# Kernel tuning notes

Measured on AMD Instinct MI355X. Metric: run time of the kernel, lower is better.

The kernel has to match this reference:

```python
import jax, jax.numpy as jnp
import numpy as np

EPS = 1e-6

def rmsnorm(x, w):
    # x: (B, N, D), w: (D,)
    var = jnp.mean(jnp.square(x), axis=-1, keepdims=True)
    return x * jax.lax.rsqrt(var + EPS) * w

def head_mixing(x):
    # Parameter-free cross-head mix: split each head's D dims into N chunks
    # and transpose the (head, chunk) axes. x: (B, N, D), D % N == 0.
    B, N, D = x.shape
    c = D // N
    return x.reshape(B, N, N, c).transpose(0, 2, 1, 3).reshape(B, N, D)

def setup_inputs() -> dict:
    key = jax.random.key(0)
    ks = jax.random.split(key, 4)
    B, N, D, H = 8192, 16, 256, 512
    return {
        "x": jax.random.normal(ks[0], (B, N, D), dtype=jnp.float32),
        "norm1_w": jnp.ones((D,), dtype=jnp.float32),
        "norm2_w": jnp.ones((D,), dtype=jnp.float32),
        "w1": jax.random.normal(ks[1], (N, D, H), dtype=jnp.float32) * (1.0 / np.sqrt(D)),
        "w3": jax.random.normal(ks[2], (N, D, H), dtype=jnp.float32) * (1.0 / np.sqrt(D)),
        "w2": jax.random.normal(ks[3], (N, H, D), dtype=jnp.float32) * (1.0 / np.sqrt(H)),
    }

def reference(x, norm1_w, norm2_w, w1, w3, w2):
    # P = HeadMixing(RMSNorm(X)) + X
    p = head_mixing(rmsnorm(x, norm1_w)) + x
    # Q = PerHeadSwiGLUFFN(RMSNorm(P)) + P  (grouped per-head SwiGLU)
    pn = rmsnorm(p, norm2_w)                       # (B, N, D)
    g = jnp.einsum('bnd,ndh->bnh', pn, w1)         # gate proj
    u = jnp.einsum('bnd,ndh->bnh', pn, w3)         # up proj
    h = jax.nn.silu(g) * u                         # (B, N, H)
    q = jnp.einsum('bnh,nhd->bnd', h, w2) + p
    return q
```

## Files before the change

kernel.cpp:

```cpp
#include <hip/hip_runtime.h>
#include <hip/hip_bf16.h>

#define B_ 8192
#define N_ 16
#define D_ 256
#define H_ 512

using bf16x8 = __attribute__((ext_vector_type(8))) short;
using f32x4  = __attribute__((ext_vector_type(4))) float;

__device__ __forceinline__ void gload_lds16(const void* g, void* l) {
    __builtin_amdgcn_global_load_lds(
        (const __attribute__((address_space(1))) void*)g,
        (__attribute__((address_space(3))) void*)l, 16, 0, 0);
}

__device__ __forceinline__ short f2bf(float f) {
    unsigned int u = __float_as_uint(f);
    u += 0x7fffu + ((u >> 16) & 1u);
    return (short)(u >> 16);
}

__device__ __forceinline__ float bf2f(short s) {
    return __uint_as_float(((unsigned int)(unsigned short)s) << 16);
}

__device__ __forceinline__ unsigned int pack2(float lo, float hi) {
    return (unsigned int)(unsigned short)f2bf(lo)
         | ((unsigned int)(unsigned short)f2bf(hi) << 16);
}

__device__ __forceinline__ f32x4 mfma(bf16x8 a, bf16x8 b, f32x4 c) {
    return __builtin_amdgcn_mfma_f32_16x16x32_bf16(a, b, c, 0, 0, 0);
}

__device__ __forceinline__ bf16x8 rd64(const short* base, int row, int g) {
    int gp = (g ^ row) & 7;
    return *(const bf16x8*)&base[(row << 6) + (gp << 3)];
}

template<int NT>
__device__ __forceinline__ void gemmc(const short* __restrict__ Ag, int sA,
                                      const short* __restrict__ Bg, int sB,
                                      short* As, short* Bs,
                                      f32x4 (&acc)[4][4],
                                      int t, int rowA0, int rowB0) {
    int lane = t & 63;
    int l16 = lane & 15, kq = lane >> 4;

#pragma unroll 1
    for (int kt = 0; kt < NT; ++kt) {
        int k0 = kt * 64;
#pragma unroll
        for (int rnd = 0; rnd < 4; ++rnd) {
            int flat = rnd * 256 + t;
            int row = flat >> 3, g = flat & 7;
            int sg = (g ^ row) & 7;
            gload_lds16(Ag + (size_t)row * sA + k0 + sg * 8, As + flat * 8);
        }
#pragma unroll
        for (int rnd = 0; rnd < 4; ++rnd) {
            int flat = rnd * 256 + t;
            int row = flat >> 3, g = flat & 7;
            int sg = (g ^ row) & 7;
            gload_lds16(Bg + (size_t)row * sB + k0 + sg * 8, Bs + flat * 8);
        }
        __syncthreads();

#pragma unroll
        for (int kh = 0; kh < 2; ++kh) {
            int g = kh * 4 + kq;
            bf16x8 aF[4], bF[4];
#pragma unroll
            for (int j = 0; j < 4; ++j)
                bF[j] = rd64(Bs, rowB0 + j * 16 + l16, g);
#pragma unroll
            for (int i = 0; i < 4; ++i)
                aF[i] = rd64(As, rowA0 + i * 16 + l16, g);
#pragma unroll
            for (int i = 0; i < 4; ++i)
#pragma unroll
                for (int j = 0; j < 4; ++j)
                    acc[i][j] = mfma(aF[i], bF[j], acc[i][j]);
        }
        __syncthreads();
    }
}

__global__ __launch_bounds__(256) void k_prep(const float* __restrict__ w1,
                                              const float* __restrict__ w3,
                                              const float* __restrict__ w2,
                                              short* __restrict__ wgu,
                                              short* __restrict__ w2t) {
    int o = blockIdx.x * 256 + threadIdx.x;
    int n = o >> 17;
    int r = o & 131071;
    int h = r >> 8, d = r & 255;
    size_t base = ((size_t)n * 1024 + (h >> 4) * 32 + (h & 15)) * 256 + d;
    wgu[base]            = f2bf(w1[(size_t)n * 131072 + (size_t)d * 512 + h]);
    wgu[base + 16 * 256] = f2bf(w3[(size_t)n * 131072 + (size_t)d * 512 + h]);
    int d2 = r >> 9, h2 = r & 511;
    w2t[o] = f2bf(w2[(size_t)n * 131072 + (size_t)h2 * 256 + d2]);
}

__global__ __launch_bounds__(256) void k_mix(const float* __restrict__ x,
                                             const float* __restrict__ n1w,
                                             const float* __restrict__ n2w,
                                             unsigned int* __restrict__ pb_u,
                                             unsigned int* __restrict__ pn_u) {
    __shared__ __align__(16) float xs[N_ * D_];
    __shared__ __align__(16) float ps[N_ * D_];
    __shared__ float inv1[N_];
    __shared__ float inv2[N_];
    int b = blockIdx.x;
    int t = threadIdx.x;
    int w = t >> 6, lane = t & 63;

    const float4* xb4 = (const float4*)(x + (size_t)b * (N_ * D_));
    float4* xs4 = (float4*)xs;
    float4* ps4 = (float4*)ps;
#pragma unroll
    for (int i = 0; i < 4; ++i) xs4[t + i * 256] = xb4[t + i * 256];
    __syncthreads();

#pragma unroll
    for (int q = 0; q < 4; ++q) {
        int row = w * 4 + q;
        float4 v = xs4[row * 64 + lane];
        float s = v.x * v.x + v.y * v.y + v.z * v.z + v.w * v.w;
        s += __shfl_xor(s, 1);  s += __shfl_xor(s, 2);
        s += __shfl_xor(s, 4);  s += __shfl_xor(s, 8);
        s += __shfl_xor(s, 16); s += __shfl_xor(s, 32);
        if (lane == 0) inv1[row] = rsqrtf(s * (1.0f / 256.0f) + 1e-6f);
    }
    __syncthreads();

    {
        int n = t >> 4, j = t & 15;
        float i1 = inv1[n];
#pragma unroll 1
        for (int m = 0; m < 16; ++m) {
            float v = xs[n * 256 + m * 16 + j] * i1 * n1w[m * 16 + j]
                    + xs[m * 256 + t];
            ps[m * 256 + t] = v;
        }
    }
    __syncthreads();

#pragma unroll
    for (int q = 0; q < 4; ++q) {
        int row = w * 4 + q;
        float4 v = ps4[row * 64 + lane];
        float s = v.x * v.x + v.y * v.y + v.z * v.z + v.w * v.w;
        s += __shfl_xor(s, 1);  s += __shfl_xor(s, 2);
        s += __shfl_xor(s, 4);  s += __shfl_xor(s, 8);
        s += __shfl_xor(s, 16); s += __shfl_xor(s, 32);
        if (lane == 0) inv2[row] = rsqrtf(s * (1.0f / 256.0f) + 1e-6f);
    }
    __syncthreads();

    int dh = t & 127, mh = t >> 7;
    float wA = n2w[2 * dh], wB = n2w[2 * dh + 1];
#pragma unroll
    for (int i = 0; i < 8; ++i) {
        int m = mh * 8 + i;
        float2 f = *(const float2*)&ps[m * 256 + 2 * dh];
        float iv = inv2[m];
        size_t off = ((size_t)m * B_ + b) * (D_ / 2) + dh;
        pb_u[off] = pack2(f.x, f.y);
        pn_u[off] = pack2(f.x * iv * wA, f.y * iv * wB);
    }
}

__global__ __launch_bounds__(256, 4) void k_gu(const short* __restrict__ pn,
                                               const short* __restrict__ wgu,
                                               short* __restrict__ hact) {
    __shared__ __align__(16) short As[128 * 64];
    __shared__ __align__(16) short Bs[128 * 64];

    int bid = blockIdx.x;
    int bx = (bid & 7) * 1024 + (bid >> 3);
    int head = bx >> 9;
    int mt = (bx >> 3) & 63;
    int nt = bx & 7;

    int t = threadIdx.x;
    int w = t >> 6, lane = t & 63;
    int l16 = lane & 15, kq = lane >> 4;
    int wm = w >> 1, wn = w & 1;

    f32x4 acc[4][4];
#pragma unroll
    for (int i = 0; i < 4; ++i)
#pragma unroll
        for (int j = 0; j < 4; ++j) acc[i][j] = (f32x4){0.f, 0.f, 0.f, 0.f};

    const short* Ag = pn  + ((size_t)head * B_ + (size_t)mt * 128) * D_;
    const short* Bg = wgu + ((size_t)head * 1024 + (size_t)nt * 128) * D_;

    gemmc<4>(Ag, D_, Bg, D_, As, Bs, acc, t, wm * 64, wn * 64);

    size_t hb = (size_t)head * B_ * H_;
#pragma unroll
    for (int mf = 0; mf < 4; ++mf) {
        int m = mt * 128 + wm * 64 + mf * 16 + kq * 4;
#pragma unroll
        for (int p = 0; p < 2; ++p) {
            int h = nt * 64 + (wn * 2 + p) * 16 + l16;
#pragma unroll
            for (int r = 0; r < 4; ++r) {
                float g = acc[mf][2 * p][r];
                float u = acc[mf][2 * p + 1][r];
                float hv = g * (1.0f / (1.0f + __expf(-g))) * u;
                hact[hb + (size_t)(m + r) * H_ + h] = f2bf(hv);
            }
        }
    }
}

__global__ __launch_bounds__(256, 4) void k_dn(const short* __restrict__ hact,
                                               const short* __restrict__ w2t,
                                               const short* __restrict__ pb,
                                               float* __restrict__ out) {
    __shared__ __align__(16) short As[128 * 64];
    __shared__ __align__(16) short Bs[128 * 64];

    int bid = blockIdx.x;
    int bx = (bid & 7) * 256 + (bid >> 3);
    int head = bx >> 7;
    int mt = (bx >> 1) & 63;
    int nt = bx & 1;

    int t = threadIdx.x;
    int w = t >> 6, lane = t & 63;
    int l16 = lane & 15, kq = lane >> 4;
    int wm = w >> 1, wn = w & 1;

    f32x4 acc[4][4];
#pragma unroll
    for (int i = 0; i < 4; ++i)
#pragma unroll
        for (int j = 0; j < 4; ++j) acc[i][j] = (f32x4){0.f, 0.f, 0.f, 0.f};

    const short* Ag = hact + ((size_t)head * B_ + (size_t)mt * 128) * H_;
    const short* Bg = w2t  + ((size_t)head * D_ + (size_t)nt * 128) * H_;

    gemmc<8>(Ag, H_, Bg, H_, As, Bs, acc, t, wm * 64, wn * 64);

#pragma unroll
    for (int mf = 0; mf < 4; ++mf) {
        int m = mt * 128 + wm * 64 + mf * 16 + kq * 4;
#pragma unroll
        for (int nf = 0; nf < 4; ++nf) {
            int d = nt * 128 + wn * 64 + nf * 16 + l16;
#pragma unroll
            for (int r = 0; r < 4; ++r) {
                float v = acc[mf][nf][r]
                        + bf2f(pb[((size_t)head * B_ + m + r) * D_ + d]);
                out[(size_t)(m + r) * (N_ * D_) + head * D_ + d] = v;
            }
        }
    }
}

extern "C" void kernel_launch(void* const* d_in, const int* in_sizes, int n_in,
                              void* d_out, int out_size, void* d_ws, size_t ws_size,
                              hipStream_t stream) {
    const float* x   = (const float*)d_in[0];
    const float* n1w = (const float*)d_in[1];
    const float* n2w = (const float*)d_in[2];
    const float* w1  = (const float*)d_in[3];
    const float* w3  = (const float*)d_in[4];
    const float* w2  = (const float*)d_in[5];
    float* out = (float*)d_out;

    char* ws = (char*)d_ws;
    short* wgu  = (short*)(ws);
    short* w2t  = (short*)(ws + (8ull   << 20));
    short* pn   = (short*)(ws + (12ull  << 20));
    short* pb   = (short*)(ws + (76ull  << 20));
    short* hact = (short*)(ws + (140ull << 20));

    k_prep<<<(N_ * D_ * H_) / 256, 256, 0, stream>>>(w1, w3, w2, wgu, w2t);
    k_mix<<<B_, 256, 0, stream>>>(x, n1w, n2w,
                                  (unsigned int*)pb, (unsigned int*)pn);
    k_gu<<<N_ * (B_ / 128) * (1024 / 128), 256, 0, stream>>>(pn, wgu, hact);
    k_dn<<<N_ * (B_ / 128) * (D_ / 128), 256, 0, stream>>>(hact, w2t, pb, out);
}
```

Before: 286.0 us.

## Keep A tile resident in k_gu, double-buffer k_dn, stagger mix LDS access

k_gu now loads the full 128x256 activation tile into LDS once and loops over all 8 N-tiles of the gate/up weights, so the A operand is not re-fetched per output tile. k_dn gets double-buffered LDS staging so the next K-slice's global loads overlap the current MFMAs. k_mix rotates its chunk index per thread group to reduce LDS bank conflicts. Dynamic LDS grows to 80KB and 64KB, and launch bounds drop to 2 blocks per CU, which lowers occupancy and cuts k_gu's grid to 1024 blocks, each running a serial loop.

```diff
diff --git a/kernel.cpp b/kernel.cpp
--- a/kernel.cpp
+++ b/kernel.cpp
@@ -34,56 +34,21 @@
     return __builtin_amdgcn_mfma_f32_16x16x32_bf16(a, b, c, 0, 0, 0);
 }
 
-__device__ __forceinline__ bf16x8 rd64(const short* base, int row, int g) {
-    int gp = (g ^ row) & 7;
-    return *(const bf16x8*)&base[(row << 6) + (gp << 3)];
-}
-
-template<int NT>
-__device__ __forceinline__ void gemmc(const short* __restrict__ Ag, int sA,
-                                      const short* __restrict__ Bg, int sB,
-                                      short* As, short* Bs,
-                                      f32x4 (&acc)[4][4],
-                                      int t, int rowA0, int rowB0) {
-    int lane = t & 63;
-    int l16 = lane & 15, kq = lane >> 4;
-
-#pragma unroll 1
-    for (int kt = 0; kt < NT; ++kt) {
-        int k0 = kt * 64;
-#pragma unroll
-        for (int rnd = 0; rnd < 4; ++rnd) {
-            int flat = rnd * 256 + t;
-            int row = flat >> 3, g = flat & 7;
-            int sg = (g ^ row) & 7;
-            gload_lds16(Ag + (size_t)row * sA + k0 + sg * 8, As + flat * 8);
-        }
-#pragma unroll
-        for (int rnd = 0; rnd < 4; ++rnd) {
-            int flat = rnd * 256 + t;
-            int row = flat >> 3, g = flat & 7;
-            int sg = (g ^ row) & 7;
-            gload_lds16(Bg + (size_t)row * sB + k0 + sg * 8, Bs + flat * 8);
-        }
-        __syncthreads();
-
-#pragma unroll
-        for (int kh = 0; kh < 2; ++kh) {
-            int g = kh * 4 + kq;
-            bf16x8 aF[4], bF[4];
-#pragma unroll
-            for (int j = 0; j < 4; ++j)
-                bF[j] = rd64(Bs, rowB0 + j * 16 + l16, g);
-#pragma unroll
-            for (int i = 0; i < 4; ++i)
-                aF[i] = rd64(As, rowA0 + i * 16 + l16, g);
-#pragma unroll
-            for (int i = 0; i < 4; ++i)
-#pragma unroll
-                for (int j = 0; j < 4; ++j)
-                    acc[i][j] = mfma(aF[i], bF[j], acc[i][j]);
-        }
-        __syncthreads();
+template<int GR>
+__device__ __forceinline__ bf16x8 rdg(const short* base, int row, int g) {
+    int gp = (g & ~7) | ((g ^ row) & 7);
+    return *(const bf16x8*)&base[row * GR * 8 + gp * 8];
+}
+
+template<int S>
+__device__ __forceinline__ void stage64(const short* __restrict__ gsrc, int k0,
+                                        short* lds, int t) {
+#pragma unroll
+    for (int rnd = 0; rnd < 4; ++rnd) {
+        int flat = rnd * 256 + t;
+        int row = flat >> 3, g = flat & 7;
+        int sg = (g ^ row) & 7;
+        gload_lds16(gsrc + (size_t)row * S + k0 + sg * 8, lds + flat * 8);
     }
 }
 
@@ -140,9 +105,10 @@
         float i1 = inv1[n];
 #pragma unroll 1
         for (int m = 0; m < 16; ++m) {
-            float v = xs[n * 256 + m * 16 + j] * i1 * n1w[m * 16 + j]
-                    + xs[m * 256 + t];
-            ps[m * 256 + t] = v;
+            int mm = (m + n) & 15;
+            float v = xs[n * 256 + mm * 16 + j] * i1 * n1w[mm * 16 + j]
+                    + xs[mm * 256 + t];
+            ps[mm * 256 + t] = v;
         }
     }
     __syncthreads();
@@ -172,58 +138,93 @@
     }
 }
 
-__global__ __launch_bounds__(256, 4) void k_gu(const short* __restrict__ pn,
+__global__ __launch_bounds__(256, 2) void k_gu(const short* __restrict__ pn,
                                                const short* __restrict__ wgu,
                                                short* __restrict__ hact) {
-    __shared__ __align__(16) short As[128 * 64];
-    __shared__ __align__(16) short Bs[128 * 64];
+    extern __shared__ short sm[];
+    short* As = sm;
+    short* Bs = sm + 32768;
 
     int bid = blockIdx.x;
-    int bx = (bid & 7) * 1024 + (bid >> 3);
-    int head = bx >> 9;
-    int mt = (bx >> 3) & 63;
-    int nt = bx & 7;
+    int bx = (bid & 7) * 128 + (bid >> 3);
+    int head = bx >> 6;
+    int mt = bx & 63;
 
     int t = threadIdx.x;
     int w = t >> 6, lane = t & 63;
     int l16 = lane & 15, kq = lane >> 4;
     int wm = w >> 1, wn = w & 1;
-
-    f32x4 acc[4][4];
-#pragma unroll
-    for (int i = 0; i < 4; ++i)
-#pragma unroll
-        for (int j = 0; j < 4; ++j) acc[i][j] = (f32x4){0.f, 0.f, 0.f, 0.f};
-
-    const short* Ag = pn  + ((size_t)head * B_ + (size_t)mt * 128) * D_;
-    const short* Bg = wgu + ((size_t)head * 1024 + (size_t)nt * 128) * D_;
-
-    gemmc<4>(Ag, D_, Bg, D_, As, Bs, acc, t, wm * 64, wn * 64);
+    int rowA0 = wm * 64, rowB0 = wn * 64;
+
+    const short* Ag = pn + ((size_t)head * B_ + (size_t)mt * 128) * D_;
+
+#pragma unroll
+    for (int rnd = 0; rnd < 16; ++rnd) {
+        int flat = rnd * 256 + t;
+        int row = flat >> 5, g = flat & 31;
+        int sg = (g & ~7) | ((g ^ row) & 7);
+        gload_lds16(Ag + (size_t)row * D_ + sg * 8, As + flat * 8);
+    }
 
     size_t hb = (size_t)head * B_ * H_;
-#pragma unroll
-    for (int mf = 0; mf < 4; ++mf) {
-        int m = mt * 128 + wm * 64 + mf * 16 + kq * 4;
-#pragma unroll
-        for (int p = 0; p < 2; ++p) {
-            int h = nt * 64 + (wn * 2 + p) * 16 + l16;
-#pragma unroll
-            for (int r = 0; r < 4; ++r) {
-                float g = acc[mf][2 * p][r];
-                float u = acc[mf][2 * p + 1][r];
-                float hv = g * (1.0f / (1.0f + __expf(-g))) * u;
-                hact[hb + (size_t)(m + r) * H_ + h] = f2bf(hv);
+
+#pragma unroll 1
+    for (int nt = 0; nt < 8; ++nt) {
+        const short* Bg = wgu + ((size_t)head * 1024 + (size_t)nt * 128) * D_;
+
+        f32x4 acc[4][4];
+#pragma unroll
+        for (int i = 0; i < 4; ++i)
+#pragma unroll
+            for (int j = 0; j < 4; ++j) acc[i][j] = (f32x4){0.f, 0.f, 0.f, 0.f};
+
+#pragma unroll
+        for (int kt = 0; kt < 4; ++kt) {
+            stage64<256>(Bg, kt * 64, Bs, t);
+            __syncthreads();
+#pragma unroll
+            for (int kh = 0; kh < 2; ++kh) {
+                int gB = kh * 4 + kq;
+                int gA = kt * 8 + kh * 4 + kq;
+                bf16x8 aF[4], bF[4];
+#pragma unroll
+                for (int j = 0; j < 4; ++j)
+                    bF[j] = rdg<8>(Bs, rowB0 + j * 16 + l16, gB);
+#pragma unroll
+                for (int i = 0; i < 4; ++i)
+                    aF[i] = rdg<32>(As, rowA0 + i * 16 + l16, gA);
+#pragma unroll
+                for (int i = 0; i < 4; ++i)
+#pragma unroll
+                    for (int j = 0; j < 4; ++j)
+                        acc[i][j] = mfma(aF[i], bF[j], acc[i][j]);
             }
-        }
-    }
-}
-
-__global__ __launch_bounds__(256, 4) void k_dn(const short* __restrict__ hact,
+            __syncthreads();
+        }
+
+#pragma unroll
+        for (int mf = 0; mf < 4; ++mf) {
+            int m = mt * 128 + wm * 64 + mf * 16 + kq * 4;
+#pragma unroll
+            for (int p = 0; p < 2; ++p) {
+                int h = nt * 64 + (wn * 2 + p) * 16 + l16;
+#pragma unroll
+                for (int r = 0; r < 4; ++r) {
+                    float g = acc[mf][2 * p][r];
+                    float u = acc[mf][2 * p + 1][r];
+                    float hv = g * (1.0f / (1.0f + __expf(-g))) * u;
+                    hact[hb + (size_t)(m + r) * H_ + h] = f2bf(hv);
+                }
+            }
+        }
+    }
+}
+
+__global__ __launch_bounds__(256, 2) void k_dn(const short* __restrict__ hact,
                                                const short* __restrict__ w2t,
                                                const short* __restrict__ pb,
                                                float* __restrict__ out) {
-    __shared__ __align__(16) short As[128 * 64];
-    __shared__ __align__(16) short Bs[128 * 64];
+    extern __shared__ short sm[];
 
     int bid = blockIdx.x;
     int bx = (bid & 7) * 256 + (bid >> 3);
@@ -235,6 +236,7 @@
     int w = t >> 6, lane = t & 63;
     int l16 = lane & 15, kq = lane >> 4;
     int wm = w >> 1, wn = w & 1;
+    int rowA0 = wm * 64, rowB0 = wn * 64;
 
     f32x4 acc[4][4];
 #pragma unroll
@@ -245,7 +247,36 @@
     const short* Ag = hact + ((size_t)head * B_ + (size_t)mt * 128) * H_;
     const short* Bg = w2t  + ((size_t)head * D_ + (size_t)nt * 128) * H_;
 
-    gemmc<8>(Ag, H_, Bg, H_, As, Bs, acc, t, wm * 64, wn * 64);
+    stage64<512>(Ag, 0, sm, t);
+    stage64<512>(Bg, 0, sm + 16384, t);
+    __syncthreads();
+
+#pragma unroll
+    for (int kt = 0; kt < 8; ++kt) {
+        short* Asl = sm + (kt & 1) * 8192;
+        short* Bsl = sm + 16384 + (kt & 1) * 8192;
+        if (kt < 7) {
+            stage64<512>(Ag, (kt + 1) * 64, sm + ((kt + 1) & 1) * 8192, t);
+            stage64<512>(Bg, (kt + 1) * 64, sm + 16384 + ((kt + 1) & 1) * 8192, t);
+        }
+#pragma unroll
+        for (int kh = 0; kh < 2; ++kh) {
+            int g = kh * 4 + kq;
+            bf16x8 aF[4], bF[4];
+#pragma unroll
+            for (int j = 0; j < 4; ++j)
+                bF[j] = rdg<8>(Bsl, rowB0 + j * 16 + l16, g);
+#pragma unroll
+            for (int i = 0; i < 4; ++i)
+                aF[i] = rdg<8>(Asl, rowA0 + i * 16 + l16, g);
+#pragma unroll
+            for (int i = 0; i < 4; ++i)
+#pragma unroll
+                for (int j = 0; j < 4; ++j)
+                    acc[i][j] = mfma(aF[i], bF[j], acc[i][j]);
+        }
+        __syncthreads();
+    }
 
 #pragma unroll
     for (int mf = 0; mf < 4; ++mf) {
@@ -281,9 +312,14 @@
     short* pb   = (short*)(ws + (76ull  << 20));
     short* hact = (short*)(ws + (140ull << 20));
 
+    (void)hipFuncSetAttribute((const void*)k_gu,
+                              hipFuncAttributeMaxDynamicSharedMemorySize, 81920);
+    (void)hipFuncSetAttribute((const void*)k_dn,
+                              hipFuncAttributeMaxDynamicSharedMemorySize, 65536);
+
     k_prep<<<(N_ * D_ * H_) / 256, 256, 0, stream>>>(w1, w3, w2, wgu, w2t);
     k_mix<<<B_, 256, 0, stream>>>(x, n1w, n2w,
                                   (unsigned int*)pb, (unsigned int*)pn);
-    k_gu<<<N_ * (B_ / 128) * (1024 / 128), 256, 0, stream>>>(pn, wgu, hact);
-    k_dn<<<N_ * (B_ / 128) * (D_ / 128), 256, 0, stream>>>(hact, w2t, pb, out);
-}
+    k_gu<<<N_ * (B_ / 128), 256, 81920, stream>>>(pn, wgu, hact);
+    k_dn<<<N_ * (B_ / 128) * (D_ / 128), 256, 65536, stream>>>(hact, w2t, pb, out);
+}
```

Measured after the change: 318.4 us. 11.3% more time.

## Widen GEMM tiles to 128x256 with 512-thread blocks for gate-up and down projections

Applied to the files above, without the earlier changes.

Both GEMM kernels now use 512-thread blocks (8 waves) computing 128x256 output tiles instead of 256-thread blocks computing 128x128. The A tile is staged once per block and reused across twice as many output columns, halving global reads of activations and the number of blocks. The K loop is also fully unrolled with compile-time strides. LDS use grows to 48KB per block, which may lower occupancy, and the down projection grid shrinks to 1024 blocks.

```diff
diff --git a/kernel.cpp b/kernel.cpp
--- a/kernel.cpp
+++ b/kernel.cpp
@@ -34,37 +34,37 @@
     return __builtin_amdgcn_mfma_f32_16x16x32_bf16(a, b, c, 0, 0, 0);
 }
 
-__device__ __forceinline__ bf16x8 rd64(const short* base, int row, int g) {
+__device__ __forceinline__ bf16x8 rdp(const short* base, int row, int g) {
     int gp = (g ^ row) & 7;
     return *(const bf16x8*)&base[(row << 6) + (gp << 3)];
 }
 
-template<int NT>
-__device__ __forceinline__ void gemmc(const short* __restrict__ Ag, int sA,
-                                      const short* __restrict__ Bg, int sB,
+template<int ROWS, int S>
+__device__ __forceinline__ void stage512(const short* __restrict__ gsrc,
+                                         int k0, short* lds, int t) {
+#pragma unroll
+    for (int rnd = 0; rnd < ROWS / 64; ++rnd) {
+        int flat = rnd * 512 + t;
+        int row = flat >> 3, g = flat & 7;
+        int sg = (g ^ row) & 7;
+        gload_lds16(gsrc + (size_t)row * S + k0 + sg * 8, lds + flat * 8);
+    }
+}
+
+template<int NT, int SA, int SB>
+__device__ __forceinline__ void gemmw(const short* __restrict__ Ag,
+                                      const short* __restrict__ Bg,
                                       short* As, short* Bs,
                                       f32x4 (&acc)[4][4],
                                       int t, int rowA0, int rowB0) {
     int lane = t & 63;
     int l16 = lane & 15, kq = lane >> 4;
 
-#pragma unroll 1
+#pragma unroll
     for (int kt = 0; kt < NT; ++kt) {
-        int k0 = kt * 64;
-#pragma unroll
-        for (int rnd = 0; rnd < 4; ++rnd) {
-            int flat = rnd * 256 + t;
-            int row = flat >> 3, g = flat & 7;
-            int sg = (g ^ row) & 7;
-            gload_lds16(Ag + (size_t)row * sA + k0 + sg * 8, As + flat * 8);
-        }
-#pragma unroll
-        for (int rnd = 0; rnd < 4; ++rnd) {
-            int flat = rnd * 256 + t;
-            int row = flat >> 3, g = flat & 7;
-            int sg = (g ^ row) & 7;
-            gload_lds16(Bg + (size_t)row * sB + k0 + sg * 8, Bs + flat * 8);
-        }
+        const int k0 = kt * 64;
+        stage512<128, SA>(Ag, k0, As, t);
+        stage512<256, SB>(Bg, k0, Bs, t);
         __syncthreads();
 
 #pragma unroll
@@ -73,10 +73,10 @@
             bf16x8 aF[4], bF[4];
 #pragma unroll
             for (int j = 0; j < 4; ++j)
-                bF[j] = rd64(Bs, rowB0 + j * 16 + l16, g);
+                bF[j] = rdp(Bs, rowB0 + j * 16 + l16, g);
 #pragma unroll
             for (int i = 0; i < 4; ++i)
-                aF[i] = rd64(As, rowA0 + i * 16 + l16, g);
+                aF[i] = rdp(As, rowA0 + i * 16 + l16, g);
 #pragma unroll
             for (int i = 0; i < 4; ++i)
 #pragma unroll
@@ -172,22 +172,22 @@
     }
 }
 
-__global__ __launch_bounds__(256, 4) void k_gu(const short* __restrict__ pn,
+__global__ __launch_bounds__(512, 4) void k_gu(const short* __restrict__ pn,
                                                const short* __restrict__ wgu,
                                                short* __restrict__ hact) {
     __shared__ __align__(16) short As[128 * 64];
-    __shared__ __align__(16) short Bs[128 * 64];
+    __shared__ __align__(16) short Bs[256 * 64];
 
     int bid = blockIdx.x;
-    int bx = (bid & 7) * 1024 + (bid >> 3);
-    int head = bx >> 9;
-    int mt = (bx >> 3) & 63;
-    int nt = bx & 7;
+    int bx = (bid & 7) * 512 + (bid >> 3);
+    int head = bx >> 8;
+    int mt = (bx >> 2) & 63;
+    int nt2 = bx & 3;
 
     int t = threadIdx.x;
     int w = t >> 6, lane = t & 63;
     int l16 = lane & 15, kq = lane >> 4;
-    int wm = w >> 1, wn = w & 1;
+    int wm = w >> 2, wn = w & 3;
 
     f32x4 acc[4][4];
 #pragma unroll
@@ -196,9 +196,9 @@
         for (int j = 0; j < 4; ++j) acc[i][j] = (f32x4){0.f, 0.f, 0.f, 0.f};
 
     const short* Ag = pn  + ((size_t)head * B_ + (size_t)mt * 128) * D_;
-    const short* Bg = wgu + ((size_t)head * 1024 + (size_t)nt * 128) * D_;
-
-    gemmc<4>(Ag, D_, Bg, D_, As, Bs, acc, t, wm * 64, wn * 64);
+    const short* Bg = wgu + ((size_t)head * 1024 + (size_t)nt2 * 256) * D_;
+
+    gemmw<4, D_, D_>(Ag, Bg, As, Bs, acc, t, wm * 64, wn * 64);
 
     size_t hb = (size_t)head * B_ * H_;
 #pragma unroll
@@ -206,7 +206,7 @@
         int m = mt * 128 + wm * 64 + mf * 16 + kq * 4;
 #pragma unroll
         for (int p = 0; p < 2; ++p) {
-            int h = nt * 64 + (wn * 2 + p) * 16 + l16;
+            int h = (nt2 * 8 + wn * 2 + p) * 16 + l16;
 #pragma unroll
             for (int r = 0; r < 4; ++r) {
                 float g = acc[mf][2 * p][r];
@@ -218,23 +218,22 @@
     }
 }
 
-__global__ __launch_bounds__(256, 4) void k_dn(const short* __restrict__ hact,
+__global__ __launch_bounds__(512, 4) void k_dn(const short* __restrict__ hact,
                                                const short* __restrict__ w2t,
                                                const short* __restrict__ pb,
                                                float* __restrict__ out) {
     __shared__ __align__(16) short As[128 * 64];
-    __shared__ __align__(16) short Bs[128 * 64];
+    __shared__ __align__(16) short Bs[256 * 64];
 
     int bid = blockIdx.x;
-    int bx = (bid & 7) * 256 + (bid >> 3);
-    int head = bx >> 7;
-    int mt = (bx >> 1) & 63;
-    int nt = bx & 1;
+    int bx = (bid & 7) * 128 + (bid >> 3);
+    int head = bx >> 6;
+    int mt = bx & 63;
 
     int t = threadIdx.x;
     int w = t >> 6, lane = t & 63;
     int l16 = lane & 15, kq = lane >> 4;
-    int wm = w >> 1, wn = w & 1;
+    int wm = w >> 2, wn = w & 3;
 
     f32x4 acc[4][4];
 #pragma unroll
@@ -243,16 +242,16 @@
         for (int j = 0; j < 4; ++j) acc[i][j] = (f32x4){0.f, 0.f, 0.f, 0.f};
 
     const short* Ag = hact + ((size_t)head * B_ + (size_t)mt * 128) * H_;
-    const short* Bg = w2t  + ((size_t)head * D_ + (size_t)nt * 128) * H_;
-
-    gemmc<8>(Ag, H_, Bg, H_, As, Bs, acc, t, wm * 64, wn * 64);
+    const short* Bg = w2t  + (size_t)head * D_ * H_;
+
+    gemmw<8, H_, H_>(Ag, Bg, As, Bs, acc, t, wm * 64, wn * 64);
 
 #pragma unroll
     for (int mf = 0; mf < 4; ++mf) {
         int m = mt * 128 + wm * 64 + mf * 16 + kq * 4;
 #pragma unroll
         for (int nf = 0; nf < 4; ++nf) {
-            int d = nt * 128 + wn * 64 + nf * 16 + l16;
+            int d = wn * 64 + nf * 16 + l16;
 #pragma unroll
             for (int r = 0; r < 4; ++r) {
                 float v = acc[mf][nf][r]
@@ -284,6 +283,6 @@
     k_prep<<<(N_ * D_ * H_) / 256, 256, 0, stream>>>(w1, w3, w2, wgu, w2t);
     k_mix<<<B_, 256, 0, stream>>>(x, n1w, n2w,
                                   (unsigned int*)pb, (unsigned int*)pn);
-    k_gu<<<N_ * (B_ / 128) * (1024 / 128), 256, 0, stream>>>(pn, wgu, hact);
-    k_dn<<<N_ * (B_ / 128) * (D_ / 128), 256, 0, stream>>>(hact, w2t, pb, out);
-}
+    k_gu<<<N_ * (B_ / 128) * 4, 512, 0, stream>>>(pn, wgu, hact);
+    k_dn<<<N_ * (B_ / 128), 512, 0, stream>>>(hact, w2t, pb, out);
+}
```

After: 326.7 us. 14.3% more time.
